# Kernel tuning notes

Hardware: AMD Instinct MI355X
Metric: run time of the kernel (lower is better)

The kernel has to match this reference:

```python
import jax, jax.numpy as jnp
import numpy as np
from jax import lax

B, CIN, HC, D, H, W = 4, 16, 16, 31, 128, 128


def setup_inputs() -> dict:
    key = jax.random.key(0)
    k1, k2, k3, k4, k5 = jax.random.split(key, 5)
    inputs = jax.random.normal(k1, (B, CIN, D, H, W), dtype=jnp.float32)
    # Conv3d weight: [out=2*HC, in=CIN, 3,3,3]
    conv_w = jax.random.normal(k2, (2 * HC, CIN, 3, 3, 3), dtype=jnp.float32) * 0.05
    # FFN weights stored as [in, out] (equivalent to torch Linear weight.T)
    w1 = jax.random.normal(k3, (HC, 2 * HC), dtype=jnp.float32) * 0.1
    w2 = jax.random.normal(k4, (2 * HC, HC), dtype=jnp.float32) * 0.1
    w3 = jax.random.normal(k5, (HC, 2 * HC), dtype=jnp.float32) * 0.1
    return {"inputs": inputs, "conv_w": conv_w, "w1": w1, "w2": w2, "w3": w3,
            "reverse": 0}


def reference(inputs, conv_w, w1, w2, w3, reverse):
    hc = conv_w.shape[0] // 2
    # 3D conv producing 2*hc gate channels  [B, 2hc, D, H, W]
    gates = lax.conv_general_dilated(
        inputs, conv_w, window_strides=(1, 1, 1), padding='SAME',
        dimension_numbers=('NCDHW', 'OIDHW', 'NCDHW'))
    Z = jnp.tanh(gates[:, :hc])            # [B, hc, D, H, W]
    F = jax.nn.sigmoid(gates[:, hc:])
    # scan over depth (spectral) dim; h0 = 0 reproduces h = (1-f)*z at step 0
    Zs = jnp.moveaxis(Z, 2, 0)             # [D, B, hc, H, W]
    Fs = jnp.moveaxis(F, 2, 0)
    if reverse:
        Zs, Fs = Zs[::-1], Fs[::-1]

    def step(h, zf):
        z, f = zf
        h = f * h + (1.0 - f) * z
        return h, h

    h0 = jnp.zeros_like(Zs[0])
    _, hs = lax.scan(step, h0, (Zs, Fs))   # [D, B, hc, H, W]
    if reverse:
        hs = hs[::-1]
    out = jnp.moveaxis(hs, 0, 2)           # [B, hc, D, H, W]
    # channel-enhanced FFN on channel-last layout
    x = jnp.moveaxis(out, 1, -1)           # [B, D, H, W, hc]
    x1 = jnp.dot(jax.nn.gelu(jnp.dot(x, w1), approximate=False), w2)
    g = jnp.dot(x, w3)                     # [B, D, H, W, 2hc]
    a, wg = jnp.split(g, 2, axis=-1)
    y = x1 + a * jax.nn.sigmoid(wg)
    return jnp.moveaxis(y, -1, 1)          # [B, hc, D, H, W]
```

## Files before the change

### kernel.cpp

```cpp
#include <hip/hip_runtime.h>
#include <hip/hip_fp16.h>

#define HC 16
#define CIN 16
#define BD 31
#define HH 128
#define WW 128
#define PLANE (HH*WW)
#define CH_STRIDE (BD*PLANE)

typedef __attribute__((ext_vector_type(8))) short bf16x8;
typedef __attribute__((ext_vector_type(16))) float f32x16;

#define LOG2E 1.442695041f

__device__ __forceinline__ ushort f2bf(float f) {
    unsigned u = __float_as_uint(f);
    u = (u + 0x7fffu + ((u >> 16) & 1u)) >> 16;
    return (ushort)u;
}
__device__ __forceinline__ unsigned pack_bf2(float lo, float hi) {
    unsigned r;
    asm("v_cvt_pk_bf16_f32 %0, %1, %2" : "=v"(r) : "v"(lo), "v"(hi));
    return r;
}
__device__ __forceinline__ float2 sigmoid2l(float na, float nb) {
    float ea = __builtin_amdgcn_exp2f(na);
    float eb = __builtin_amdgcn_exp2f(nb);
    float pa = 1.0f + ea, pb = 1.0f + eb;
    float r  = __builtin_amdgcn_rcpf(pa * pb);
    return make_float2(pb * r, pa * r);
}
__device__ __forceinline__ float2 gelu2(float x, float y) {
    float ux = fmaf(0.044715f * x, x * x, x);
    float uy = fmaf(0.044715f * y, y * y, y);
    float ex = __builtin_amdgcn_exp2f(-2.3021841f * ux);
    float ey = __builtin_amdgcn_exp2f(-2.3021841f * uy);
    float px = 1.0f + ex, py = 1.0f + ey;
    float r  = __builtin_amdgcn_rcpf(px * py);
    return make_float2(x * py * r, y * px * r);
}

__global__ __launch_bounds__(256)
void xprep_kernel(const float* __restrict__ inp, char* __restrict__ xT,
                  const float* __restrict__ cw,
                  const float* __restrict__ w1,
                  const float* __restrict__ w2,
                  const float* __restrict__ w3,
                  ushort* __restrict__ wtab, ushort* __restrict__ wtab2)
{
    if (blockIdx.x >= 7936) {
        int idx = (blockIdx.x - 7936) * 256 + threadIdx.x;
        if (idx < 13824) {
            int j    = idx & 7;
            int lane = (idx >> 3) & 63;
            int t    = (idx >> 9) % 9;
            int kd   = (idx >> 9) / 9;
            int co = lane & 31;
            int ci = 8 * (lane >> 5) + j;
            int kh = t / 3, kw = t % 3;
            wtab[idx] = f2bf(cw[(co * CIN + ci) * 27 + kd * 9 + kh * 3 + kw]);
            return;
        }
        idx -= 13824;
        if (idx >= 2048) return;
        int e    = idx & 7;
        int lane = (idx >> 3) & 63;
        int tbl  = idx >> 9;
        int m  = lane & 31;
        int hi = lane >> 5;
        int k  = (e & 3) + 8 * (e >> 2) + 4 * hi;
        float v = 0.f;
        if (tbl == 0)      v = w1[k * 32 + m];
        else if (tbl == 3) v = w3[k * 32 + m];
        else {
            int mf = tbl - 1;
            if (m < 16) v = w2[(k + 16 * mf) * 16 + m];
        }
        wtab2[idx] = f2bf(v);
        return;
    }

    __shared__ float tile[16][256];
    int t  = threadIdx.x;
    int hp = blockIdx.x & 63;
    int g  = blockIdx.x >> 6;
    int d  = g % BD;
    int b  = g / BD;

    size_t src = (size_t)b * CIN * CH_STRIDE + (size_t)d * PLANE + hp * 256;
    #pragma unroll
    for (int c = 0; c < 16; ++c)
        tile[c][t] = inp[src + (size_t)c * CH_STRIDE + t];
    __syncthreads();

    int w  = t & 127;
    int rr = t >> 7;
    char* rowp = xT + (((size_t)(b * BD + d) * 128) + hp * 2 + rr) * 4096;
    #pragma unroll
    for (int q = 0; q < 2; ++q) {
        uint4 pk;
        pk.x = (unsigned)f2bf(tile[q*8+0][t]) | ((unsigned)f2bf(tile[q*8+1][t]) << 16);
        pk.y = (unsigned)f2bf(tile[q*8+2][t]) | ((unsigned)f2bf(tile[q*8+3][t]) << 16);
        pk.z = (unsigned)f2bf(tile[q*8+4][t]) | ((unsigned)f2bf(tile[q*8+5][t]) << 16);
        pk.w = (unsigned)f2bf(tile[q*8+6][t]) | ((unsigned)f2bf(tile[q*8+7][t]) << 16);
        unsigned off = ((unsigned)((w + 1) * 32 + q * 16) ^ (((unsigned)(w + 1) & 0xE) << 3)) - 32;
        *(uint4*)(rowp + off) = pk;
    }
}

#define SLOT_B (3 * 4224)

__device__ __forceinline__ void gload_lds16(const void* g, void* l) {
    __builtin_amdgcn_global_load_lds(
        (const __attribute__((address_space(1))) unsigned int*)g,
        (__attribute__((address_space(3))) unsigned int*)l, 16, 0, 0);
}

__global__ __launch_bounds__(256, 2)
void qrnn_fused(const char* __restrict__ xT,
                const ushort* __restrict__ wtab,
                const ushort* __restrict__ wtab2,
                float* __restrict__ out,
                const int* __restrict__ rev_p)
{
    __shared__ __align__(16) char slab[4][SLOT_B];

    int p = blockIdx.x;
    int logical = (p & 7) * 64 + (p >> 3);
    int b  = logical >> 7;
    int ht = logical & 127;
    int rev = rev_p[0];

    int lane = threadIdx.x & 63;
    int wid  = threadIdx.x >> 6;
    int wl   = lane & 31;
    int hi   = lane >> 5;
    int cio  = hi * 16;

    const bf16x8* wt = (const bf16x8*)wtab;
    bf16x8 af[27];
    #pragma unroll
    for (int t = 0; t < 27; ++t) af[t] = wt[t * 64 + lane];

    const bf16x8* W2 = (const bf16x8*)wtab2;
    bf16x8 af1  = W2[lane];
    bf16x8 af2a = W2[64 + lane];
    bf16x8 af2b = W2[128 + lane];
    bf16x8 af3  = W2[192 + lane];

    unsigned bpo[3];
    #pragma unroll
    for (int dwn = 0; dwn < 3; ++dwn) {
        unsigned wc = (unsigned)(wl + dwn);
        bpo[dwn] = (unsigned)(wid * 1024) + ((wc * 32 + cio) ^ ((wc & 0xE) << 3));
    }

    for (int i = threadIdx.x; i < 4 * 3 * 32; i += 256) {
        int s = i / 96;
        int r = (i / 32) % 3;
        int k = i & 31;
        int off = (k < 8) ? (k * 4) : (4128 + (k - 8) * 4);
        *(int*)(slab[s] + r * 4224 + off) = 0;
    }

    auto zero_slot = [&](int s) {
        for (int i = threadIdx.x; i < 768; i += 256) {
            int r = i >> 8;
            int k = i & 255;
            *(uint4*)(slab[s] + r * 4224 + 32 + k * 16) = uint4{0, 0, 0, 0};
        }
    };

    auto stage = [&](int s, int plane) {
        const char* pl = xT + ((size_t)(b * BD + plane) * 128) * 4096;
        for (int c = wid; c < 12; c += 4) {
            int rr = c >> 2, ch = c & 3;
            int h = ht - 1 + rr;
            char* dst = slab[s] + rr * 4224 + 32 + ch * 1024;
            if ((unsigned)h < (unsigned)HH)
                gload_lds16(pl + (size_t)h * 4096 + ch * 1024 + lane * 16, dst);
            else
                *(uint4*)(dst + lane * 16) = uint4{0, 0, 0, 0};
        }
    };

    f32x16 zacc;
    #pragma unroll
    for (int r = 0; r < 16; ++r) zacc[r] = 0.f;

    auto convd = [&](int d) -> f32x16 {
        f32x16 A = zacc;
        #pragma unroll
        for (int kd = 0; kd < 3; ++kd) {
            const char* sb = slab[(d - 1 + kd) & 3];
            #pragma unroll
            for (int t = 0; t < 9; ++t) {
                bf16x8 bfr = *(const bf16x8*)(sb + (t / 3) * 4224 + bpo[t % 3]);
                A = __builtin_amdgcn_mfma_f32_32x32x16_bf16(af[kd * 9 + t], bfr, A, 0, 0, 0);
            }
        }
        return A;
    };

    float h[8];
    #pragma unroll
    for (int j = 0; j < 8; ++j) h[j] = 0.f;

    float* obase = out + (size_t)b * HC * CH_STRIDE + ht * WW + wid * 32 + wl;

    auto tail = [&](const f32x16& A, int d) {
        union { bf16x8 v; unsigned u[4]; } bx;
        #pragma unroll
        for (int r = 0; r < 8; ++r) {
            float2 s = sigmoid2l(-2.0f * LOG2E * A[r], -LOG2E * A[r + 8]);
            float z = fmaf(2.0f, s.x, -1.0f);
            float f = s.y;
            h[r] = z + f * (h[r] - z);
        }
        #pragma unroll
        for (int q = 0; q < 4; ++q)
            bx.u[q] = pack_bf2(h[2 * q], h[2 * q + 1]);

        f32x16 a1 = __builtin_amdgcn_mfma_f32_32x32x16_bf16(af1, bx.v, zacc, 0, 0, 0);
        f32x16 a3 = __builtin_amdgcn_mfma_f32_32x32x16_bf16(af3, bx.v, zacc, 0, 0, 0);

        union { bf16x8 v; unsigned u[4]; } b2a, b2b;
        #pragma unroll
        for (int q = 0; q < 4; ++q) {
            float2 ga = gelu2(a1[2 * q],     a1[2 * q + 1]);
            float2 gb = gelu2(a1[8 + 2 * q], a1[8 + 2 * q + 1]);
            b2a.u[q] = pack_bf2(ga.x, ga.y);
            b2b.u[q] = pack_bf2(gb.x, gb.y);
        }
        f32x16 a2 = __builtin_amdgcn_mfma_f32_32x32x16_bf16(af2a, b2a.v, zacc, 0, 0, 0);
        a2 = __builtin_amdgcn_mfma_f32_32x32x16_bf16(af2b, b2b.v, a2, 0, 0, 0);

        float* ob = obase + (size_t)d * PLANE;
        #pragma unroll
        for (int q = 0; q < 4; ++q) {
            float2 s = sigmoid2l(-LOG2E * a3[8 + 2 * q], -LOG2E * a3[9 + 2 * q]);
            int c0 = (2 * q     & 3) + 8 * (2 * q     >> 2) + 4 * hi;
            int c1 = (2 * q + 1 & 3) + 8 * (2 * q + 1 >> 2) + 4 * hi;
            ob[(size_t)c0 * CH_STRIDE] = fmaf(a3[2 * q],     s.x, a2[2 * q]);
            ob[(size_t)c1 * CH_STRIDE] = fmaf(a3[2 * q + 1], s.y, a2[2 * q + 1]);
        }
    };

    int d0  = rev ? (BD - 1) : 0;
    int sgn = rev ? -1 : 1;
    int oobq = rev ? -1 : BD;

    stage(d0 & 3, d0);
    stage((d0 + sgn) & 3, d0 + sgn);
    zero_slot((d0 - sgn) & 3);
    __syncthreads();

    f32x16 accP;
    {
        int q = d0 + 2 * sgn;
        if (q >= 0 && q < BD) stage(q & 3, q);
        accP = convd(d0);
        __syncthreads();
    }

    #pragma unroll 1
    for (int i = 1; i < BD; ++i) {
        int d = d0 + sgn * i;
        int q = d + 2 * sgn;
        if (q >= 0 && q < BD) stage(q & 3, q);
        else if (q == oobq)   zero_slot(q & 3);

        f32x16 acc = convd(d);
        tail(accP, d - sgn);
        accP = acc;

        __syncthreads();
    }
    tail(accP, d0 + sgn * (BD - 1));
}

extern "C" void kernel_launch(void* const* d_in, const int* in_sizes, int n_in,
                              void* d_out, int out_size, void* d_ws, size_t ws_size,
                              hipStream_t stream)
{
    const float* inp = (const float*)d_in[0];
    const float* cw  = (const float*)d_in[1];
    const float* w1  = (const float*)d_in[2];
    const float* w2  = (const float*)d_in[3];
    const float* w3  = (const float*)d_in[4];
    const int*   rev = (const int*)d_in[5];

    ushort* wtab  = (ushort*)d_ws;
    ushort* wtab2 = (ushort*)((char*)d_ws + 27648);
    char*   xT    = (char*)d_ws + 32768;

    xprep_kernel<<<dim3(7998), dim3(256), 0, stream>>>(
        inp, xT, cw, w1, w2, w3, wtab, wtab2);

    qrnn_fused<<<dim3(512), dim3(256), 0, stream>>>(
        xT, wtab, wtab2, (float*)d_out, rev);
}
```

Before: 128.2 us.

## Deepen LDS ring to six slots and process two depth steps per barrier

Grows the shared-memory plane ring from four to six slots. The main loop now stages two planes ahead and runs two conv+tail steps between each __syncthreads, which halves the number of block barriers and gives global-to-LDS loads more time to land. For the reverse direction, conv weights are reordered at load time so that slot indexing runs in logical step space. The cost is about 50% more LDS per block, which could limit occupancy if the two-blocks-per-CU target no longer fits, plus extra register pressure from holding two accumulators at once.

```diff
diff --git a/kernel.cpp b/kernel.cpp
--- a/kernel.cpp
+++ b/kernel.cpp
@@ -124,13 +124,15 @@
                 float* __restrict__ out,
                 const int* __restrict__ rev_p)
 {
-    __shared__ __align__(16) char slab[4][SLOT_B];
+    __shared__ __align__(16) char slab[6][SLOT_B];
 
     int p = blockIdx.x;
     int logical = (p & 7) * 64 + (p >> 3);
     int b  = logical >> 7;
     int ht = logical & 127;
     int rev = rev_p[0];
+    int sgn = rev ? -1 : 1;
+    int d0  = rev ? (BD - 1) : 0;
 
     int lane = threadIdx.x & 63;
     int wid  = threadIdx.x >> 6;
@@ -141,7 +143,12 @@
     const bf16x8* wt = (const bf16x8*)wtab;
     bf16x8 af[27];
     #pragma unroll
-    for (int t = 0; t < 27; ++t) af[t] = wt[t * 64 + lane];
+    for (int m = 0; m < 3; ++m) {
+        int kd = rev ? (2 - m) : m;
+        #pragma unroll
+        for (int t = 0; t < 9; ++t)
+            af[m * 9 + t] = wt[(kd * 9 + t) * 64 + lane];
+    }
 
     const bf16x8* W2 = (const bf16x8*)wtab2;
     bf16x8 af1  = W2[lane];
@@ -156,7 +163,7 @@
         bpo[dwn] = (unsigned)(wid * 1024) + ((wc * 32 + cio) ^ ((wc & 0xE) << 3));
     }
 
-    for (int i = threadIdx.x; i < 4 * 3 * 32; i += 256) {
+    for (int i = threadIdx.x; i < 6 * 3 * 32; i += 256) {
         int s = i / 96;
         int r = (i / 32) % 3;
         int k = i & 31;
@@ -172,12 +179,14 @@
         }
     };
 
-    auto stage = [&](int s, int plane) {
+    auto stage = [&](int j) {
+        int plane = d0 + sgn * j;
         const char* pl = xT + ((size_t)(b * BD + plane) * 128) * 4096;
+        char* sb = slab[j % 6];
         for (int c = wid; c < 12; c += 4) {
             int rr = c >> 2, ch = c & 3;
             int h = ht - 1 + rr;
-            char* dst = slab[s] + rr * 4224 + 32 + ch * 1024;
+            char* dst = sb + rr * 4224 + 32 + ch * 1024;
             if ((unsigned)h < (unsigned)HH)
                 gload_lds16(pl + (size_t)h * 4096 + ch * 1024 + lane * 16, dst);
             else
@@ -189,15 +198,15 @@
     #pragma unroll
     for (int r = 0; r < 16; ++r) zacc[r] = 0.f;
 
-    auto convd = [&](int d) -> f32x16 {
+    auto convd = [&](int j) -> f32x16 {
         f32x16 A = zacc;
         #pragma unroll
-        for (int kd = 0; kd < 3; ++kd) {
-            const char* sb = slab[(d - 1 + kd) & 3];
+        for (int m = 0; m < 3; ++m) {
+            const char* sb = slab[(j - 1 + m + 6) % 6];
             #pragma unroll
             for (int t = 0; t < 9; ++t) {
                 bf16x8 bfr = *(const bf16x8*)(sb + (t / 3) * 4224 + bpo[t % 3]);
-                A = __builtin_amdgcn_mfma_f32_32x32x16_bf16(af[kd * 9 + t], bfr, A, 0, 0, 0);
+                A = __builtin_amdgcn_mfma_f32_32x32x16_bf16(af[m * 9 + t], bfr, A, 0, 0, 0);
             }
         }
         return A;
@@ -247,33 +256,26 @@
         }
     };
 
-    int d0  = rev ? (BD - 1) : 0;
-    int sgn = rev ? -1 : 1;
-    int oobq = rev ? -1 : BD;
-
-    stage(d0 & 3, d0);
-    stage((d0 + sgn) & 3, d0 + sgn);
-    zero_slot((d0 - sgn) & 3);
+    zero_slot(5);
+    stage(0); stage(1); stage(2); stage(3);
     __syncthreads();
 
-    f32x16 accP;
-    {
-        int q = d0 + 2 * sgn;
-        if (q >= 0 && q < BD) stage(q & 3, q);
-        accP = convd(d0);
-        __syncthreads();
-    }
+    f32x16 accP = convd(0);
+    __syncthreads();
 
     #pragma unroll 1
-    for (int i = 1; i < BD; ++i) {
-        int d = d0 + sgn * i;
-        int q = d + 2 * sgn;
-        if (q >= 0 && q < BD) stage(q & 3, q);
-        else if (q == oobq)   zero_slot(q & 3);
-
-        f32x16 acc = convd(d);
-        tail(accP, d - sgn);
-        accP = acc;
+    for (int i = 1; i < BD; i += 2) {
+        int js0 = i + 3, js1 = i + 4;
+        if (js0 <= BD - 1) stage(js0);
+        else if (js0 == BD) zero_slot(js0 % 6);
+        if (js1 <= BD - 1) stage(js1);
+        else if (js1 == BD) zero_slot(js1 % 6);
+
+        f32x16 a0 = convd(i);
+        tail(accP, d0 + sgn * (i - 1));
+        f32x16 a1 = convd(i + 1);
+        tail(a0, d0 + sgn * i);
+        accP = a1;
 
         __syncthreads();
     }
```

New measurement: 130.6 us. About the same (+1.8%).
